# Kernel optimization log

Hardware: AMD Instinct MI355X
Metric: run time of the kernel (lower is better)

The kernel has to match this reference:

```python
import jax, jax.numpy as jnp
import numpy as np

C = 32
RES = 512
LEVEL = 6
RADIUS = 2  # half-width of specular filtering window per mip level
_lev_res = [RES >> i for i in range(LEVEL)]
_offsets = np.concatenate([[0], np.cumsum([r * r for r in _lev_res])]).astype(np.int32)
TOTAL = int(_offsets[-1])
_roughness = np.linspace(0.03, 0.99, LEVEL).astype(np.float32)


def _face_dirs(R):
    # unit direction of each texel center on each of the 6 cube faces: (6,R,R,3)
    t = ((np.arange(R) + 0.5) / R * 2.0 - 1.0).astype(np.float32)
    vv, uu = np.meshgrid(t, t, indexing='ij')  # vv: rows (v), uu: cols (u)
    one = np.ones_like(uu)
    f = np.stack([
        np.stack([one, -vv, -uu], -1),   # +x
        np.stack([-one, -vv, uu], -1),   # -x
        np.stack([uu, one, vv], -1),     # +y
        np.stack([uu, -one, -vv], -1),   # -y
        np.stack([uu, -vv, one], -1),    # +z
        np.stack([-uu, -vv, -one], -1)], 0)  # -z
    return (f / np.linalg.norm(f, axis=-1, keepdims=True)).astype(np.float32)

_DIRS = [jnp.asarray(_face_dirs(r)) for r in _lev_res]


def _ggx(cos, alpha):
    a2 = alpha * alpha
    d = a2 / (np.pi * (cos * cos * (a2 - 1.0) + 1.0) ** 2)
    return jnp.where(cos > 0, d, 0.0)


def _specular_filter(feat, dirs, rough):
    # GGX-weighted neighborhood filtering per texel (bounded window = 'specular bound')
    R = feat.shape[-1]
    alpha = float(rough) ** 2
    idx = jnp.arange(R)
    fsum = jnp.zeros_like(feat)
    wsum = jnp.zeros(feat.shape[1:], dtype=feat.dtype)  # (6,R,R)
    for di in range(-RADIUS, RADIUS + 1):
        ii = jnp.clip(idx + di, 0, R - 1)
        for dj in range(-RADIUS, RADIUS + 1):
            jj = jnp.clip(idx + dj, 0, R - 1)
            nd = dirs[:, ii][:, :, jj]                    # (6,R,R,3)
            cos = jnp.clip((dirs * nd).sum(-1), -1.0, 1.0)
            wgt = _ggx(cos, alpha)                        # (6,R,R)
            fsum = fsum + feat[:, :, ii][:, :, :, jj] * wgt[None]
            wsum = wsum + wgt
    return fsum / jnp.maximum(wsum, 1e-8)[None]


def _avg_pool2(x):
    Cc, F, R, _ = x.shape
    return x.reshape(Cc, F, R // 2, 2, R // 2, 2).mean(axis=(3, 5))


def _create_mip(feature):
    pools = [feature.reshape(C, 6, -1)]
    feat = feature
    for i in range(1, LEVEL):
        feat = _avg_pool2(feat)
        pools.append(_specular_filter(feat, _DIRS[i], float(_roughness[i])).reshape(C, 6, -1))
    return jnp.concatenate(pools, axis=-1)  # (C, 6, TOTAL)


def _fetch(mip_pool, w, r):
    # w in [0,1] encodes direction d = 2w-1; pick major-axis cube face, bilinear in face,
    # linear across mip levels selected by roughness r.
    d = w * 2.0 - 1.0
    d = d / jnp.linalg.norm(d, axis=-1, keepdims=True)
    dx, dy, dz = d[:, 0], d[:, 1], d[:, 2]
    ax, ay, az = jnp.abs(dx), jnp.abs(dy), jnp.abs(dz)
    condx = (ax >= ay) & (ax >= az)
    condy = (ay >= az) & (~condx)
    ma = jnp.where(condx, ax, jnp.where(condy, ay, az))
    face = jnp.where(condx, jnp.where(dx > 0, 0, 1),
           jnp.where(condy, jnp.where(dy > 0, 2, 3), jnp.where(dz > 0, 4, 5)))
    u = jnp.where(condx, jnp.where(dx > 0, -dz, dz),
        jnp.where(condy, dx, jnp.where(dz > 0, dx, -dx))) / ma
    v = jnp.where(condx, -dy, jnp.where(condy, jnp.where(dy > 0, dz, -dz), -dy)) / ma
    u01 = (u + 1.0) * 0.5
    v01 = (v + 1.0) * 0.5
    lev_f = jnp.clip((r - _roughness[0]) / (_roughness[-1] - _roughness[0]), 0.0, 1.0) * (LEVEL - 1)
    l0 = jnp.clip(jnp.floor(lev_f).astype(jnp.int32), 0, LEVEL - 1)
    l1 = jnp.minimum(l0 + 1, LEVEL - 1)
    t = lev_f - l0.astype(lev_f.dtype)
    offs = jnp.asarray(_offsets)
    pool_flat = mip_pool.reshape(C, 6 * TOTAL)
    fbase = face.astype(jnp.int32) * TOTAL

    def sample(l):
        res_l = (RES // jnp.left_shift(1, l)).astype(jnp.int32)  # per-query level res
        rf = res_l.astype(u01.dtype)
        x = jnp.clip(u01 * rf - 0.5, 0.0, rf - 1.0)
        y = jnp.clip(v01 * rf - 0.5, 0.0, rf - 1.0)
        x0 = jnp.floor(x).astype(jnp.int32)
        y0 = jnp.floor(y).astype(jnp.int32)
        x1 = jnp.minimum(x0 + 1, res_l - 1)
        y1 = jnp.minimum(y0 + 1, res_l - 1)
        fx = x - x0
        fy = y - y0
        base = fbase + offs[l]
        def g(yy, xx):
            return jnp.take(pool_flat, base + yy * res_l + xx, axis=1)  # (C,B)
        return (g(y0, x0) * (1 - fx) * (1 - fy) + g(y0, x1) * fx * (1 - fy)
              + g(y1, x0) * (1 - fx) * fy + g(y1, x1) * fx * fy)

    out = sample(l0) * (1 - t) + sample(l1) * t  # (C,B)
    return out.T  # (B,C)


def setup_inputs() -> dict:
    key = jax.random.key(0)
    k1, k2, k3 = jax.random.split(key, 3)
    B = 262144
    feature = jax.random.normal(k1, (C, 6, RES, RES), dtype=jnp.float32) * 0.1
    w = jax.random.uniform(k2, (B, 3), dtype=jnp.float32)
    r = jax.random.uniform(k3, (B,), dtype=jnp.float32)
    return {"feature": feature, "w": w, "r": r}


def reference(feature, w, r):
    mip_pool = _create_mip(feature)
    return _fetch(mip_pool, w, r)
```

## Files before the change

### kernel.cpp

```cpp
#include <hip/hip_runtime.h>
#include <cstddef>

#define PI_F 3.14159265358979323846f
#define TOTAL_TEX 349440
#define NC 32
#define LP 257

__constant__ int c_offs[6] = {0, 262144, 327680, 344064, 348160, 349184};

static __device__ inline unsigned int f2bf(float x) {
  union { float f; unsigned int u; } v; v.f = x;
  return (v.u + 0x7FFFu + ((v.u >> 16) & 1u)) >> 16;
}
static __device__ inline unsigned int pack2(float lo, float hi) {
  return f2bf(lo) | (f2bf(hi) << 16);
}
static __device__ inline float4 bf4(uint2 q) {
  union { unsigned int u; float f; } a;
  float4 r;
  a.u = q.x << 16;          r.x = a.f;
  a.u = q.x & 0xFFFF0000u;  r.y = a.f;
  a.u = q.y << 16;          r.z = a.f;
  a.u = q.y & 0xFFFF0000u;  r.w = a.f;
  return r;
}

__global__ __launch_bounds__(256) void k_transpose_pool(
    const float* __restrict__ feat, unsigned short* __restrict__ pool0,
    float* __restrict__ pooled1)
{
  __shared__ float tile[32 * LP];
  int blk = blockIdx.x;
  int tx = blk & 7;
  int rem = blk >> 3;
  int ty = rem & 127;
  int f = rem >> 7;
  int gx0 = tx << 6, gy0 = ty << 2;
  int tid = threadIdx.x;
  int lx = tid & 63, ly = tid >> 6;
  int pix = ly * 64 + lx;

  const float* fp = feat + ((size_t)f * 512 + (gy0 + ly)) * 512 + gx0 + lx;
#pragma unroll
  for (int c = 0; c < 32; ++c) {
    tile[c * LP + pix] = fp[(size_t)c * (6 * 512 * 512)];
  }
  __syncthreads();

  size_t rowbase = ((size_t)f * TOTAL_TEX + (size_t)gy0 * 512 + gx0) * NC;
#pragma unroll
  for (int it = 0; it < 8; ++it) {
    int q = it * 256 + tid;
    int texel = q >> 3, cg = q & 7;
    int tyy = texel >> 6, txx = texel & 63;
    float v0 = tile[(cg * 4 + 0) * LP + texel];
    float v1 = tile[(cg * 4 + 1) * LP + texel];
    float v2 = tile[(cg * 4 + 2) * LP + texel];
    float v3 = tile[(cg * 4 + 3) * LP + texel];
    uint2 pk; pk.x = pack2(v0, v1); pk.y = pack2(v2, v3);
    *(uint2*)(pool0 + rowbase + ((size_t)tyy * 512 + txx) * NC + cg * 4) = pk;
  }

  size_t pbase = ((size_t)f * 65536 + (size_t)(gy0 >> 1) * 256 + (gx0 >> 1)) * NC;
#pragma unroll
  for (int it = 0; it < 8; ++it) {
    int e = it * 256 + tid;
    int c = e & 31, px = (e >> 5) & 31, py = e >> 10;
    int b0 = (2 * py) * 64 + 2 * px;
    float v = 0.25f * ((tile[c * LP + b0] + tile[c * LP + b0 + 1]) +
                       (tile[c * LP + b0 + 64] + tile[c * LP + b0 + 65]));
    pooled1[pbase + ((size_t)py * 256 + px) * NC + c] = v;
  }
}

__global__ __launch_bounds__(256) void k_pool(
    const float* __restrict__ in, float* __restrict__ out,
    int Rin, int logRout, int n)
{
  int t = blockIdx.x * 256 + threadIdx.x;
  if (t >= n) return;
  int c = t & 31;
  int rem = t >> 5;
  int Rout = Rin >> 1;
  int x = rem & (Rout - 1);
  rem >>= logRout;
  int y = rem & (Rout - 1);
  int f = rem >> logRout;
  size_t b = (((size_t)f * Rin + 2 * y) * Rin + 2 * x) * NC + c;
  size_t rowstep = (size_t)Rin * NC;
  out[t] = 0.25f * ((in[b] + in[b + NC]) + (in[b + rowstep] + in[b + rowstep + NC]));
}

__device__ inline float3 face_dir_norm(int f, int i, int j, float inv2R)
{
  float u = ((float)j + 0.5f) * inv2R - 1.0f;
  float v = ((float)i + 0.5f) * inv2R - 1.0f;
  float x, y, z;
  switch (f) {
    case 0: x = 1.0f;  y = -v; z = -u;   break;
    case 1: x = -1.0f; y = -v; z = u;    break;
    case 2: x = u;  y = 1.0f;  z = v;    break;
    case 3: x = u;  y = -1.0f; z = -v;   break;
    case 4: x = u;  y = -v;    z = 1.0f; break;
    default: x = -u; y = -v;   z = -1.0f; break;
  }
  float s = 1.0f / sqrtf(x * x + y * y + z * z);
  float3 o; o.x = x * s; o.y = y * s; o.z = z * s;
  return o;
}

__global__ __launch_bounds__(256) void k_filter2(
    const float* __restrict__ in, unsigned short* __restrict__ out,
    int R, int logR, float a2)
{
  __shared__ float wlds[32 * 26];
  int tid = threadIdx.x;
  int p0 = blockIdx.x << 5;
  float inv2R = 2.0f / (float)R;

  {
    int pl = tid & 31;
    int tg = tid >> 5;
    int p = p0 + pl;
    int j = p & (R - 1);
    int i = (p >> logR) & (R - 1);
    int f = p >> (2 * logR);
    float3 dc = face_dir_norm(f, i, j, inv2R);
    for (int tap = tg; tap < 25; tap += 8) {
      int di = tap / 5 - 2;
      int dj = tap - (tap / 5) * 5 - 2;
      int ii = min(max(i + di, 0), R - 1);
      int jj = min(max(j + dj, 0), R - 1);
      float3 dn = face_dir_norm(f, ii, jj, inv2R);
      float cs = dc.x * dn.x + dc.y * dn.y + dc.z * dn.z;
      cs = fminf(fmaxf(cs, -1.0f), 1.0f);
      float den = cs * cs * (a2 - 1.0f) + 1.0f;
      float w = (cs > 0.0f) ? (a2 / (PI_F * den * den)) : 0.0f;
      wlds[pl * 26 + tap] = w;
    }
  }
  __syncthreads();

  int cg = tid & 7;
  int pl = tid >> 3;
  int p = p0 + pl;
  int j = p & (R - 1);
  int i = (p >> logR) & (R - 1);
  int f = p >> (2 * logR);
  const float4* fbase = (const float4*)(in + (((size_t)f << (2 * logR)) * NC));

  float4 acc; acc.x = acc.y = acc.z = acc.w = 0.0f;
  float wsum = 0.0f;
#pragma unroll
  for (int di = -2; di <= 2; ++di) {
    int ii = min(max(i + di, 0), R - 1);
    int rowb = ii * R;
#pragma unroll
    for (int dj = -2; dj <= 2; ++dj) {
      int jj = min(max(j + dj, 0), R - 1);
      int tap = (di + 2) * 5 + (dj + 2);
      float w = wlds[pl * 26 + tap];
      wsum += w;
      float4 v = fbase[(size_t)(rowb + jj) * 8 + cg];
      acc.x += w * v.x; acc.y += w * v.y; acc.z += w * v.z; acc.w += w * v.w;
    }
  }
  float s = 1.0f / fmaxf(wsum, 1e-8f);
  uint2 pk;
  pk.x = pack2(acc.x * s, acc.y * s);
  pk.y = pack2(acc.z * s, acc.w * s);
  ((uint2*)(out + ((size_t)f * TOTAL_TEX + (size_t)(i * R + j)) * NC))[cg] = pk;
}

__global__ __launch_bounds__(256) void k_fetch2(
    const unsigned short* __restrict__ pool, const float* __restrict__ wv,
    const float* __restrict__ rv, float* __restrict__ out, int B)
{
  int t = blockIdx.x * 256 + threadIdx.x;
  int cg = t & 7;
  int b = t >> 3;
  if (b >= B) return;

  float dx = wv[3 * b + 0] * 2.0f - 1.0f;
  float dy = wv[3 * b + 1] * 2.0f - 1.0f;
  float dz = wv[3 * b + 2] * 2.0f - 1.0f;
  float ax = fabsf(dx), ay = fabsf(dy), az = fabsf(dz);
  bool condx = (ax >= ay) && (ax >= az);
  bool condy = (ay >= az) && !condx;
  float ma = condx ? ax : (condy ? ay : az);
  int face = condx ? (dx > 0.0f ? 0 : 1)
                   : (condy ? (dy > 0.0f ? 2 : 3) : (dz > 0.0f ? 4 : 5));
  float un = condx ? (dx > 0.0f ? -dz : dz)
                   : (condy ? dx : (dz > 0.0f ? dx : -dx));
  float vn = condx ? -dy : (condy ? (dy > 0.0f ? dz : -dz) : -dy);
  float u01 = (un / ma + 1.0f) * 0.5f;
  float v01 = (vn / ma + 1.0f) * 0.5f;

  float rr = rv[b];
  float lev_f = fminf(fmaxf((rr - 0.03f) / (0.99f - 0.03f), 0.0f), 1.0f) * 5.0f;
  int l0 = (int)floorf(lev_f);
  l0 = min(max(l0, 0), 5);
  int l1 = min(l0 + 1, 5);
  float tt = lev_f - (float)l0;

  float4 acc; acc.x = acc.y = acc.z = acc.w = 0.0f;
  int   lvs[2] = {l0, l1};
  float lws[2] = {1.0f - tt, tt};
#pragma unroll
  for (int s = 0; s < 2; ++s) {
    int l = lvs[s];
    float wl = lws[s];
    int res = 512 >> l;
    float rf = (float)res;
    float x = fminf(fmaxf(u01 * rf - 0.5f, 0.0f), rf - 1.0f);
    float y = fminf(fmaxf(v01 * rf - 0.5f, 0.0f), rf - 1.0f);
    int x0 = (int)floorf(x), y0 = (int)floorf(y);
    int x1 = min(x0 + 1, res - 1), y1 = min(y0 + 1, res - 1);
    float fx = x - (float)x0, fy = y - (float)y0;
    const uint2* base8 =
        (const uint2*)(pool + ((size_t)face * TOTAL_TEX + c_offs[l]) * NC);
    float w00 = wl * (1.0f - fx) * (1.0f - fy);
    float w01 = wl * fx * (1.0f - fy);
    float w10 = wl * (1.0f - fx) * fy;
    float w11 = wl * fx * fy;
    float4 a = bf4(base8[(size_t)(y0 * res + x0) * 8 + cg]);
    float4 bq = bf4(base8[(size_t)(y0 * res + x1) * 8 + cg]);
    float4 cq = bf4(base8[(size_t)(y1 * res + x0) * 8 + cg]);
    float4 dq = bf4(base8[(size_t)(y1 * res + x1) * 8 + cg]);
    acc.x += w00 * a.x + w01 * bq.x + w10 * cq.x + w11 * dq.x;
    acc.y += w00 * a.y + w01 * bq.y + w10 * cq.y + w11 * dq.y;
    acc.z += w00 * a.z + w01 * bq.z + w10 * cq.z + w11 * dq.z;
    acc.w += w00 * a.w + w01 * bq.w + w10 * cq.w + w11 * dq.w;
  }
  ((float4*)(out + (size_t)b * NC))[cg] = acc;
}

extern "C" void kernel_launch(void* const* d_in, const int* in_sizes, int n_in,
                              void* d_out, int out_size, void* d_ws, size_t ws_size,
                              hipStream_t stream)
{
  const float* feat = (const float*)d_in[0];
  const float* wv   = (const float*)d_in[1];
  const float* rv   = (const float*)d_in[2];
  float* out = (float*)d_out;
  int B = in_sizes[1] / 3;

  unsigned short* pool_t = (unsigned short*)d_ws;
  const size_t POOLT = (size_t)6 * TOTAL_TEX * NC;
  float* pooled1 = (float*)(pool_t + POOLT);
  float* pooled2 = pooled1 + (size_t)6 * 256 * 256 * NC;
  float* pooled3 = pooled2 + (size_t)6 * 128 * 128 * NC;
  float* pooled4 = pooled3 + (size_t)6 * 64 * 64 * NC;
  float* pooled5 = pooled4 + (size_t)6 * 32 * 32 * NC;
  float* pooled[6] = {nullptr, pooled1, pooled2, pooled3, pooled4, pooled5};
  static const int offs[6] = {0, 262144, 327680, 344064, 348160, 349184};

  hipLaunchKernelGGL(k_transpose_pool, dim3(6 * 8 * 128), dim3(256), 0, stream,
                     feat, pool_t, pooled1);

  for (int l = 2; l <= 5; ++l) {
    int Rin = 512 >> (l - 1);
    int Rout = 512 >> l;
    int logRout = 9 - l;
    int n = 6 * Rout * Rout * NC;
    hipLaunchKernelGGL(k_pool, dim3((n + 255) / 256), dim3(256), 0, stream,
                       pooled[l - 1], pooled[l], Rin, logRout, n);
  }

  for (int l = 1; l <= 5; ++l) {
    int R = 512 >> l;
    int logR = 9 - l;
    double rough_d = 0.03 + 0.192 * (double)l;
    float r32 = (float)rough_d;
    double alpha = (double)r32 * (double)r32;
    float a2 = (float)(alpha * alpha);
    int npix = 6 * R * R;
    hipLaunchKernelGGL(k_filter2, dim3(npix / 32), dim3(256), 0, stream,
                       pooled[l], pool_t + (size_t)offs[l] * NC, R, logR, a2);
  }

  hipLaunchKernelGGL(k_fetch2, dim3((B * 8 + 255) / 256), dim3(256), 0, stream,
                     pool_t, wv, rv, out, B);
}
```

Baseline: 438.2 us.

## Fuse mip pooling into filter kernel and widen fetch loads to 8 channels

Removes the separate k_pool launches. Each filter block now covers a 16x2 texel tile, reuses the center tap it already loaded, and writes the 2x2-averaged next mip level from shared memory. The fetch kernel now has each thread handle 8 channels with 16-byte bf16 loads and nontemporal stores, which halves the thread count and cuts per-sample address math. This costs an extra block barrier in the filter kernel and higher register use per thread in the fetch kernel.

```diff
diff --git a/kernel.cpp b/kernel.cpp
--- a/kernel.cpp
+++ b/kernel.cpp
@@ -5,6 +5,8 @@
 #define TOTAL_TEX 349440
 #define NC 32
 #define LP 257
+
+typedef float nf4 __attribute__((ext_vector_type(4)));
 
 __constant__ int c_offs[6] = {0, 262144, 327680, 344064, 348160, 349184};
 
@@ -23,6 +25,13 @@
   a.u = q.y << 16;          r.z = a.f;
   a.u = q.y & 0xFFFF0000u;  r.w = a.f;
   return r;
+}
+static __device__ inline void bf8(uint4 q, float4& lo, float4& hi) {
+  uint2 a, b;
+  a.x = q.x; a.y = q.y;
+  b.x = q.z; b.y = q.w;
+  lo = bf4(a);
+  hi = bf4(b);
 }
 
 __global__ __launch_bounds__(256) void k_transpose_pool(
@@ -73,24 +82,6 @@
   }
 }
 
-__global__ __launch_bounds__(256) void k_pool(
-    const float* __restrict__ in, float* __restrict__ out,
-    int Rin, int logRout, int n)
-{
-  int t = blockIdx.x * 256 + threadIdx.x;
-  if (t >= n) return;
-  int c = t & 31;
-  int rem = t >> 5;
-  int Rout = Rin >> 1;
-  int x = rem & (Rout - 1);
-  rem >>= logRout;
-  int y = rem & (Rout - 1);
-  int f = rem >> logRout;
-  size_t b = (((size_t)f * Rin + 2 * y) * Rin + 2 * x) * NC + c;
-  size_t rowstep = (size_t)Rin * NC;
-  out[t] = 0.25f * ((in[b] + in[b + NC]) + (in[b + rowstep] + in[b + rowstep + NC]));
-}
-
 __device__ inline float3 face_dir_norm(int f, int i, int j, float inv2R)
 {
   float u = ((float)j + 0.5f) * inv2R - 1.0f;
@@ -109,22 +100,27 @@
   return o;
 }
 
-__global__ __launch_bounds__(256) void k_filter2(
+__global__ __launch_bounds__(256) void k_filter3(
     const float* __restrict__ in, unsigned short* __restrict__ out,
+    float* __restrict__ pooled_out,
     int R, int logR, float a2)
 {
   __shared__ float wlds[32 * 26];
+  __shared__ float4 clds[32][8];
   int tid = threadIdx.x;
-  int p0 = blockIdx.x << 5;
   float inv2R = 2.0f / (float)R;
+
+  int txi = blockIdx.x & ((R >> 4) - 1);
+  int rest = blockIdx.x >> (logR - 4);
+  int tyi = rest & ((R >> 1) - 1);
+  int f = rest >> (logR - 1);
+  int jbase = txi << 4, ibase = tyi << 1;
 
   {
     int pl = tid & 31;
     int tg = tid >> 5;
-    int p = p0 + pl;
-    int j = p & (R - 1);
-    int i = (p >> logR) & (R - 1);
-    int f = p >> (2 * logR);
+    int j = jbase + (pl & 15);
+    int i = ibase + (pl >> 4);
     float3 dc = face_dir_norm(f, i, j, inv2R);
     for (int tap = tg; tap < 25; tap += 8) {
       int di = tap / 5 - 2;
@@ -143,13 +139,12 @@
 
   int cg = tid & 7;
   int pl = tid >> 3;
-  int p = p0 + pl;
-  int j = p & (R - 1);
-  int i = (p >> logR) & (R - 1);
-  int f = p >> (2 * logR);
+  int j = jbase + (pl & 15);
+  int i = ibase + (pl >> 4);
   const float4* fbase = (const float4*)(in + (((size_t)f << (2 * logR)) * NC));
 
   float4 acc; acc.x = acc.y = acc.z = acc.w = 0.0f;
+  float4 cen; cen.x = cen.y = cen.z = cen.w = 0.0f;
   float wsum = 0.0f;
 #pragma unroll
   for (int di = -2; di <= 2; ++di) {
@@ -162,6 +157,7 @@
       float w = wlds[pl * 26 + tap];
       wsum += w;
       float4 v = fbase[(size_t)(rowb + jj) * 8 + cg];
+      if (di == 0 && dj == 0) cen = v;
       acc.x += w * v.x; acc.y += w * v.y; acc.z += w * v.z; acc.w += w * v.w;
     }
   }
@@ -170,15 +166,36 @@
   pk.x = pack2(acc.x * s, acc.y * s);
   pk.y = pack2(acc.z * s, acc.w * s);
   ((uint2*)(out + ((size_t)f * TOTAL_TEX + (size_t)(i * R + j)) * NC))[cg] = pk;
-}
-
-__global__ __launch_bounds__(256) void k_fetch2(
+
+  if (pooled_out) {
+    clds[pl][cg] = cen;
+    __syncthreads();
+    if (tid < 64) {
+      int m = tid >> 3;
+      int c = tid & 7;
+      float4 a = clds[0 * 16 + 2 * m][c];
+      float4 b = clds[0 * 16 + 2 * m + 1][c];
+      float4 cc = clds[16 + 2 * m][c];
+      float4 d = clds[16 + 2 * m + 1][c];
+      float4 r;
+      r.x = 0.25f * ((a.x + b.x) + (cc.x + d.x));
+      r.y = 0.25f * ((a.y + b.y) + (cc.y + d.y));
+      r.z = 0.25f * ((a.z + b.z) + (cc.z + d.z));
+      r.w = 0.25f * ((a.w + b.w) + (cc.w + d.w));
+      int Rp = R >> 1;
+      ((float4*)(pooled_out +
+                 (((size_t)f * Rp + tyi) * Rp + (txi * 8 + m)) * NC))[c] = r;
+    }
+  }
+}
+
+__global__ __launch_bounds__(256) void k_fetch4(
     const unsigned short* __restrict__ pool, const float* __restrict__ wv,
     const float* __restrict__ rv, float* __restrict__ out, int B)
 {
   int t = blockIdx.x * 256 + threadIdx.x;
-  int cg = t & 7;
-  int b = t >> 3;
+  int cg = t & 3;
+  int b = t >> 2;
   if (b >= B) return;
 
   float dx = wv[3 * b + 0] * 2.0f - 1.0f;
@@ -203,7 +220,8 @@
   int l1 = min(l0 + 1, 5);
   float tt = lev_f - (float)l0;
 
-  float4 acc; acc.x = acc.y = acc.z = acc.w = 0.0f;
+  float4 accA; accA.x = accA.y = accA.z = accA.w = 0.0f;
+  float4 accB; accB.x = accB.y = accB.z = accB.w = 0.0f;
   int   lvs[2] = {l0, l1};
   float lws[2] = {1.0f - tt, tt};
 #pragma unroll
@@ -217,22 +235,35 @@
     int x0 = (int)floorf(x), y0 = (int)floorf(y);
     int x1 = min(x0 + 1, res - 1), y1 = min(y0 + 1, res - 1);
     float fx = x - (float)x0, fy = y - (float)y0;
-    const uint2* base8 =
-        (const uint2*)(pool + ((size_t)face * TOTAL_TEX + c_offs[l]) * NC);
+    const uint4* base16 =
+        (const uint4*)(pool + ((size_t)face * TOTAL_TEX + c_offs[l]) * NC);
     float w00 = wl * (1.0f - fx) * (1.0f - fy);
     float w01 = wl * fx * (1.0f - fy);
     float w10 = wl * (1.0f - fx) * fy;
     float w11 = wl * fx * fy;
-    float4 a = bf4(base8[(size_t)(y0 * res + x0) * 8 + cg]);
-    float4 bq = bf4(base8[(size_t)(y0 * res + x1) * 8 + cg]);
-    float4 cq = bf4(base8[(size_t)(y1 * res + x0) * 8 + cg]);
-    float4 dq = bf4(base8[(size_t)(y1 * res + x1) * 8 + cg]);
-    acc.x += w00 * a.x + w01 * bq.x + w10 * cq.x + w11 * dq.x;
-    acc.y += w00 * a.y + w01 * bq.y + w10 * cq.y + w11 * dq.y;
-    acc.z += w00 * a.z + w01 * bq.z + w10 * cq.z + w11 * dq.z;
-    acc.w += w00 * a.w + w01 * bq.w + w10 * cq.w + w11 * dq.w;
-  }
-  ((float4*)(out + (size_t)b * NC))[cg] = acc;
+    uint4 qa = base16[(size_t)(y0 * res + x0) * 4 + cg];
+    uint4 qb = base16[(size_t)(y0 * res + x1) * 4 + cg];
+    uint4 qc = base16[(size_t)(y1 * res + x0) * 4 + cg];
+    uint4 qd = base16[(size_t)(y1 * res + x1) * 4 + cg];
+    float4 lo, hi;
+    bf8(qa, lo, hi);
+    accA.x += w00 * lo.x; accA.y += w00 * lo.y; accA.z += w00 * lo.z; accA.w += w00 * lo.w;
+    accB.x += w00 * hi.x; accB.y += w00 * hi.y; accB.z += w00 * hi.z; accB.w += w00 * hi.w;
+    bf8(qb, lo, hi);
+    accA.x += w01 * lo.x; accA.y += w01 * lo.y; accA.z += w01 * lo.z; accA.w += w01 * lo.w;
+    accB.x += w01 * hi.x; accB.y += w01 * hi.y; accB.z += w01 * hi.z; accB.w += w01 * hi.w;
+    bf8(qc, lo, hi);
+    accA.x += w10 * lo.x; accA.y += w10 * lo.y; accA.z += w10 * lo.z; accA.w += w10 * lo.w;
+    accB.x += w10 * hi.x; accB.y += w10 * hi.y; accB.z += w10 * hi.z; accB.w += w10 * hi.w;
+    bf8(qd, lo, hi);
+    accA.x += w11 * lo.x; accA.y += w11 * lo.y; accA.z += w11 * lo.z; accA.w += w11 * lo.w;
+    accB.x += w11 * hi.x; accB.y += w11 * hi.y; accB.z += w11 * hi.z; accB.w += w11 * hi.w;
+  }
+  nf4* o = (nf4*)(out + (size_t)b * NC);
+  nf4 va = {accA.x, accA.y, accA.z, accA.w};
+  nf4 vb = {accB.x, accB.y, accB.z, accB.w};
+  __builtin_nontemporal_store(va, o + cg * 2);
+  __builtin_nontemporal_store(vb, o + cg * 2 + 1);
 }
 
 extern "C" void kernel_launch(void* const* d_in, const int* in_sizes, int n_in,
@@ -258,15 +289,6 @@
   hipLaunchKernelGGL(k_transpose_pool, dim3(6 * 8 * 128), dim3(256), 0, stream,
                      feat, pool_t, pooled1);
 
-  for (int l = 2; l <= 5; ++l) {
-    int Rin = 512 >> (l - 1);
-    int Rout = 512 >> l;
-    int logRout = 9 - l;
-    int n = 6 * Rout * Rout * NC;
-    hipLaunchKernelGGL(k_pool, dim3((n + 255) / 256), dim3(256), 0, stream,
-                       pooled[l - 1], pooled[l], Rin, logRout, n);
-  }
-
   for (int l = 1; l <= 5; ++l) {
     int R = 512 >> l;
     int logR = 9 - l;
@@ -275,10 +297,11 @@
     double alpha = (double)r32 * (double)r32;
     float a2 = (float)(alpha * alpha);
     int npix = 6 * R * R;
-    hipLaunchKernelGGL(k_filter2, dim3(npix / 32), dim3(256), 0, stream,
-                       pooled[l], pool_t + (size_t)offs[l] * NC, R, logR, a2);
-  }
-
-  hipLaunchKernelGGL(k_fetch2, dim3((B * 8 + 255) / 256), dim3(256), 0, stream,
+    float* pout = (l < 5) ? pooled[l + 1] : nullptr;
+    hipLaunchKernelGGL(k_filter3, dim3(npix / 32), dim3(256), 0, stream,
+                       pooled[l], pool_t + (size_t)offs[l] * NC, pout, R, logR, a2);
+  }
+
+  hipLaunchKernelGGL(k_fetch4, dim3((B * 4 + 255) / 256), dim3(256), 0, stream,
                      pool_t, wv, rv, out, B);
 }
```

Result: faster. 422.8 us (-3.5%).
